# Optimization experiments

Measured on AMD Instinct MI355X. Metric: run time of the kernel, lower is better.

Reference implementation:

```python
import jax, jax.numpy as jnp
import numpy as np

EPS = 1e-5  # BatchNorm eps (torch default)


def setup_inputs() -> dict:
    key = jax.random.key(0)
    ks = jax.random.split(key, 12)
    C, Ci, B, H, W = 64, 32, 2, 96, 96  # plane, inter_plane=plane//2

    def n(k, shape, s=0.05):
        return jax.random.normal(k, shape, jnp.float32) * s

    return {
        "xA": jax.random.normal(ks[0], (B, C, H, W), jnp.float32),
        "xB": jax.random.normal(ks[1], (B, C, H, W), jnp.float32),
        "Wk": n(ks[2], (Ci, C)), "bk": n(ks[3], (Ci,)),
        "Wv": n(ks[4], (Ci, C)), "bv": n(ks[5], (Ci,)),
        "Wq": n(ks[6], (Ci, C)), "bq": n(ks[7], (Ci,)),
        "Wg": n(ks[8], (Ci, Ci)),  # conv_wg, 1x1 Conv1d, no bias
        "g1_gamma": jnp.ones((Ci,), jnp.float32), "g1_beta": jnp.zeros((Ci,), jnp.float32),
        "g1_mean": jnp.zeros((Ci,), jnp.float32), "g1_var": jnp.ones((Ci,), jnp.float32),
        "Wo": n(ks[9], (C, Ci)), "bo": n(ks[10], (C,)),
        "g2_gamma": jnp.ones((C,), jnp.float32), "g2_beta": jnp.zeros((C,), jnp.float32),
        "g2_mean": jnp.zeros((C,), jnp.float32), "g2_var": jnp.ones((C,), jnp.float32),
    }


def reference(xA, xB, Wk, bk, Wv, bv, Wq, bq, Wg,
              g1_gamma, g1_beta, g1_mean, g1_var,
              Wo, bo, g2_gamma, g2_beta, g2_mean, g2_var):
    B, C, H, W = xB.shape
    N = H * W
    # 1x1 conv2d projections -> [B, Ci, N]
    k = (jnp.einsum('bchw,oc->bohw', xA, Wk) + bk[None, :, None, None]).reshape(B, -1, N)
    v = (jnp.einsum('bchw,oc->bohw', xA, Wv) + bv[None, :, None, None]).reshape(B, -1, N)
    q = (jnp.einsum('bchw,oc->bohw', xB, Wq) + bq[None, :, None, None]).reshape(B, -1, N)
    # AV = softmax(v^T @ q, axis=2)  -> [B, N, N]
    A = jax.nn.softmax(jnp.einsum('bcn,bcm->bnm', v, q), axis=2)
    # k @ AV -> [B, Ci, N]
    av = jnp.einsum('bcn,bnm->bcm', k, A)
    # conv_wg (1x1 conv1d, no bias) + BatchNorm1d (inference form)
    av = jnp.einsum('oc,bcn->bon', Wg, av)
    av = (av - g1_mean[None, :, None]) * (g1_gamma / jnp.sqrt(g1_var + EPS))[None, :, None] + g1_beta[None, :, None]
    av = av.reshape(B, -1, H, W)
    # out: 1x1 conv2d -> plane, BatchNorm2d, residual, relu
    o = jnp.einsum('oc,bchw->bohw', Wo, av) + bo[None, :, None, None]
    o = (o - g2_mean[None, :, None, None]) * (g2_gamma / jnp.sqrt(g2_var + EPS))[None, :, None, None] + g2_beta[None, :, None, None]
    return jax.nn.relu(o + xB)
```

## Files before the change

kernel.cpp:

```cpp
#include <hip/hip_runtime.h>
#include <hip/hip_bf16.h>

#define CI 32
#define CC 64
#define NBATCH 2
#define NPIX 9216
#define NSD 24
#define LOG2E 1.4426950408889634f

typedef __attribute__((ext_vector_type(8))) short s16x8;
typedef __attribute__((ext_vector_type(4))) short s16x4;
typedef __attribute__((ext_vector_type(4))) float f32x4;
typedef __attribute__((ext_vector_type(2))) unsigned int u32x2;
typedef __attribute__((ext_vector_type(4))) unsigned int u32x4;

static __device__ __forceinline__ unsigned cvtpk(float a, float b) {
    unsigned d;
    asm("v_cvt_pk_bf16_f32 %0, %1, %2" : "=v"(d) : "v"(a), "v"(b));
    return d;
}
static __device__ __forceinline__ short f2b(float f) {
    union { float f; unsigned u; } v; v.f = f;
    return (short)((v.u + 0x7FFFu + ((v.u >> 16) & 1u)) >> 16);
}
static __device__ __forceinline__ float b2f(short s) {
    union { unsigned u; float f; } v; v.u = ((unsigned)(unsigned short)s) << 16;
    return v.f;
}
static __device__ __forceinline__ s16x8 asS16x8(u32x4 v) {
    union { u32x4 u; s16x8 s; } c; c.u = v; return c.s;
}

__global__ __launch_bounds__(256) void k_proj(
    const float* __restrict__ xA, const float* __restrict__ xB,
    const float* __restrict__ Wk, const float* __restrict__ bk,
    const float* __restrict__ Wv, const float* __restrict__ bv,
    const float* __restrict__ Wq, const float* __restrict__ bq,
    short* __restrict__ vT, short* __restrict__ qT, short* __restrict__ kC)
{
    int mode = blockIdx.y;
    const float* W    = mode == 0 ? Wk : (mode == 1 ? Wv : Wq);
    const float* bias = mode == 0 ? bk : (mode == 1 ? bv : bq);
    const float* X    = mode == 2 ? xB : xA;

    __shared__ float sW[CI * CC];
    __shared__ float sb[CI];
    __shared__ float spart[3][64][33];
    for (int i = threadIdx.x; i < CI * CC; i += 256) sW[i] = W[i];
    if (threadIdx.x < CI) sb[threadIdx.x] = bias[threadIdx.x];
    __syncthreads();

    int q4 = threadIdx.x >> 6;
    int lp = threadIdx.x & 63;
    int idx = blockIdx.x * 64 + lp;
    int b = idx / NPIX, n = idx % NPIX;

    float acc[CI];
    #pragma unroll
    for (int o = 0; o < CI; o++) acc[o] = 0.f;

    const float* px = X + (size_t)b * CC * NPIX + n;
    #pragma unroll
    for (int cc = 0; cc < 16; cc++) {
        int c = q4 * 16 + cc;
        float x = px[(size_t)c * NPIX];
        #pragma unroll
        for (int o = 0; o < CI; o++) acc[o] += sW[o * CC + c] * x;
    }
    if (q4) {
        #pragma unroll
        for (int o = 0; o < CI; o++) spart[q4 - 1][lp][o] = acc[o];
    }
    __syncthreads();
    if (q4 == 0) {
        #pragma unroll
        for (int o = 0; o < CI; o++)
            acc[o] += spart[0][lp][o] + spart[1][lp][o] + spart[2][lp][o] + sb[o];
        if (mode == 0) {
            #pragma unroll
            for (int o = 0; o < CI; o++)
                kC[((size_t)b * CI + o) * NPIX + n] = f2b(acc[o]);
        } else {
            float sc = (mode == 2) ? LOG2E : 1.0f;
            short* dst = (mode == 1 ? vT : qT) + ((size_t)b * NPIX + n) * CI;
            #pragma unroll
            for (int v4 = 0; v4 < 4; v4++) {
                u32x4 pk;
                #pragma unroll
                for (int j = 0; j < 4; j++)
                    pk[j] = cvtpk(acc[v4 * 8 + 2 * j] * sc, acc[v4 * 8 + 2 * j + 1] * sc);
                ((u32x4*)dst)[v4] = pk;
            }
        }
    }
}

__global__ __launch_bounds__(64) void k_denom(
    const short* __restrict__ vT, const short* __restrict__ qT,
    float* __restrict__ sum_part)
{
    int lane = threadIdx.x;
    int r = lane & 15, g = lane >> 4;
    int b = blockIdx.y;
    int nb = blockIdx.x * 32;

    const short* vb = vT + (size_t)b * NPIX * CI;
    s16x8 a0 = *(const s16x8*)(vb + (size_t)(nb + r) * CI + 8 * g);
    s16x8 a1 = *(const s16x8*)(vb + (size_t)(nb + 16 + r) * CI + 8 * g);

    f32x4 s0 = {0.f, 0.f, 0.f, 0.f}, s1 = {0.f, 0.f, 0.f, 0.f};
    f32x4 z  = {0.f, 0.f, 0.f, 0.f};
    const short* qb = qT + (size_t)b * NPIX * CI;
    int mlo = blockIdx.z * (NPIX / NSD);
    int mhi = mlo + NPIX / NSD;

    s16x8 q0 = *(const s16x8*)(qb + (size_t)(mlo + r) * CI + 8 * g);
    s16x8 q1 = *(const s16x8*)(qb + (size_t)(mlo + 16 + r) * CI + 8 * g);
    for (int m0 = mlo; m0 < mhi; m0 += 32) {
        int np = (m0 + 32 < mhi) ? m0 + 32 : mlo;
        s16x8 nq0 = *(const s16x8*)(qb + (size_t)(np + r) * CI + 8 * g);
        s16x8 nq1 = *(const s16x8*)(qb + (size_t)(np + 16 + r) * CI + 8 * g);

        f32x4 t00 = __builtin_amdgcn_mfma_f32_16x16x32_bf16(a0, q0, z, 0, 0, 0);
        f32x4 t01 = __builtin_amdgcn_mfma_f32_16x16x32_bf16(a0, q1, z, 0, 0, 0);
        f32x4 t10 = __builtin_amdgcn_mfma_f32_16x16x32_bf16(a1, q0, z, 0, 0, 0);
        f32x4 t11 = __builtin_amdgcn_mfma_f32_16x16x32_bf16(a1, q1, z, 0, 0, 0);
        #pragma unroll
        for (int e = 0; e < 4; e++) {
            s0[e] += __builtin_amdgcn_exp2f(t00[e]) + __builtin_amdgcn_exp2f(t01[e]);
            s1[e] += __builtin_amdgcn_exp2f(t10[e]) + __builtin_amdgcn_exp2f(t11[e]);
        }
        q0 = nq0; q1 = nq1;
    }
    #pragma unroll
    for (int mask = 1; mask < 16; mask <<= 1) {
        #pragma unroll
        for (int e = 0; e < 4; e++) {
            s0[e] += __shfl_xor(s0[e], mask, 64);
            s1[e] += __shfl_xor(s1[e], mask, 64);
        }
    }
    if (r == 0) {
        float* sp = sum_part + ((size_t)blockIdx.z * NBATCH + b) * NPIX;
        #pragma unroll
        for (int e = 0; e < 4; e++) {
            sp[nb + 4 * g + e]      = s0[e];
            sp[nb + 16 + 4 * g + e] = s1[e];
        }
    }
}

__global__ __launch_bounds__(256) void k_invd(
    const float* __restrict__ sum_part, float* __restrict__ invd)
{
    int idx = blockIdx.x * 256 + threadIdx.x;
    float s = 0.f;
    #pragma unroll
    for (int zz = 0; zz < NSD; zz++)
        s += sum_part[(size_t)zz * NBATCH * NPIX + idx];
    invd[idx] = 1.0f / s;
}

__global__ __launch_bounds__(256) void k_scale(
    short* __restrict__ kC, const float* __restrict__ invd)
{
    int idx = blockIdx.x * 256 + threadIdx.x;
    int n = idx % NPIX;
    int b = idx / (CI * NPIX);
    kC[idx] = f2b(b2f(kC[idx]) * invd[b * NPIX + n]);
}

__global__ __launch_bounds__(64) void k_attn(
    const short* __restrict__ vT, const short* __restrict__ qT,
    const short* __restrict__ kC, short* __restrict__ avp, int slice)
{
    __shared__ short plds[32][36];
    int lane = threadIdx.x;
    int r = lane & 15, g = lane >> 4;
    int b = blockIdx.y;
    int m0 = blockIdx.x * 32;

    const short* qb = qT + (size_t)b * NPIX * CI;
    s16x8 qb0 = *(const s16x8*)(qb + (size_t)(m0 + r) * CI + 8 * g);
    s16x8 qb1 = *(const s16x8*)(qb + (size_t)(m0 + 16 + r) * CI + 8 * g);

    const short* vb = vT + (size_t)b * NPIX * CI;
    const short* k0 = kC + ((size_t)b * CI + r) * NPIX;
    const short* k1 = k0 + (size_t)16 * NPIX;

    f32x4 acc00 = {0,0,0,0}, acc01 = {0,0,0,0}, acc10 = {0,0,0,0}, acc11 = {0,0,0,0};
    f32x4 z = {0,0,0,0};

    int nlo = blockIdx.z * slice;
    int nhi = nlo + slice;

    s16x8 a0  = *(const s16x8*)(vb + (size_t)(nlo + r) * CI + 8 * g);
    s16x8 a1  = *(const s16x8*)(vb + (size_t)(nlo + 16 + r) * CI + 8 * g);
    s16x8 ka0 = *(const s16x8*)(k0 + nlo + 8 * g);
    s16x8 ka1 = *(const s16x8*)(k1 + nlo + 8 * g);

    for (int n0 = nlo; n0 < nhi; n0 += 32) {
        int np = (n0 + 32 < nhi) ? n0 + 32 : nlo;
        s16x8 na0  = *(const s16x8*)(vb + (size_t)(np + r) * CI + 8 * g);
        s16x8 na1  = *(const s16x8*)(vb + (size_t)(np + 16 + r) * CI + 8 * g);
        s16x8 nka0 = *(const s16x8*)(k0 + np + 8 * g);
        s16x8 nka1 = *(const s16x8*)(k1 + np + 8 * g);

        f32x4 t00 = __builtin_amdgcn_mfma_f32_16x16x32_bf16(a0, qb0, z, 0, 0, 0);
        f32x4 t01 = __builtin_amdgcn_mfma_f32_16x16x32_bf16(a0, qb1, z, 0, 0, 0);
        f32x4 t10 = __builtin_amdgcn_mfma_f32_16x16x32_bf16(a1, qb0, z, 0, 0, 0);
        f32x4 t11 = __builtin_amdgcn_mfma_f32_16x16x32_bf16(a1, qb1, z, 0, 0, 0);

        u32x2 w00 = {cvtpk(__builtin_amdgcn_exp2f(t00[0]), __builtin_amdgcn_exp2f(t00[1])),
                     cvtpk(__builtin_amdgcn_exp2f(t00[2]), __builtin_amdgcn_exp2f(t00[3]))};
        u32x2 w10 = {cvtpk(__builtin_amdgcn_exp2f(t10[0]), __builtin_amdgcn_exp2f(t10[1])),
                     cvtpk(__builtin_amdgcn_exp2f(t10[2]), __builtin_amdgcn_exp2f(t10[3]))};
        u32x2 w01 = {cvtpk(__builtin_amdgcn_exp2f(t01[0]), __builtin_amdgcn_exp2f(t01[1])),
                     cvtpk(__builtin_amdgcn_exp2f(t01[2]), __builtin_amdgcn_exp2f(t01[3]))};
        u32x2 w11 = {cvtpk(__builtin_amdgcn_exp2f(t11[0]), __builtin_amdgcn_exp2f(t11[1])),
                     cvtpk(__builtin_amdgcn_exp2f(t11[2]), __builtin_amdgcn_exp2f(t11[3]))};

        *(u32x2*)&plds[r][4 * g]           = w00;
        *(u32x2*)&plds[r][16 + 4 * g]      = w10;
        *(u32x2*)&plds[16 + r][4 * g]      = w01;
        *(u32x2*)&plds[16 + r][16 + 4 * g] = w11;

        s16x4 l0 = *(const s16x4*)&plds[r][8 * g];
        s16x4 h0 = *(const s16x4*)&plds[r][8 * g + 4];
        s16x4 l1 = *(const s16x4*)&plds[16 + r][8 * g];
        s16x4 h1 = *(const s16x4*)&plds[16 + r][8 * g + 4];
        s16x8 pb0 = {l0[0], l0[1], l0[2], l0[3], h0[0], h0[1], h0[2], h0[3]};
        s16x8 pb1 = {l1[0], l1[1], l1[2], l1[3], h1[0], h1[1], h1[2], h1[3]};

        acc00 = __builtin_amdgcn_mfma_f32_16x16x32_bf16(ka0, pb0, acc00, 0, 0, 0);
        acc10 = __builtin_amdgcn_mfma_f32_16x16x32_bf16(ka1, pb0, acc10, 0, 0, 0);
        acc01 = __builtin_amdgcn_mfma_f32_16x16x32_bf16(ka0, pb1, acc01, 0, 0, 0);
        acc11 = __builtin_amdgcn_mfma_f32_16x16x32_bf16(ka1, pb1, acc11, 0, 0, 0);

        a0 = na0; a1 = na1; ka0 = nka0; ka1 = nka1;
    }

    short* dst = avp + ((size_t)blockIdx.z * NBATCH + b) * NPIX * CI;
    u32x2 o00 = {cvtpk(acc00[0], acc00[1]), cvtpk(acc00[2], acc00[3])};
    u32x2 o10 = {cvtpk(acc10[0], acc10[1]), cvtpk(acc10[2], acc10[3])};
    u32x2 o01 = {cvtpk(acc01[0], acc01[1]), cvtpk(acc01[2], acc01[3])};
    u32x2 o11 = {cvtpk(acc11[0], acc11[1]), cvtpk(acc11[2], acc11[3])};
    *(u32x2*)(dst + (size_t)(m0 + r) * CI + 4 * g)           = o00;
    *(u32x2*)(dst + (size_t)(m0 + r) * CI + 16 + 4 * g)      = o10;
    *(u32x2*)(dst + (size_t)(m0 + 16 + r) * CI + 4 * g)      = o01;
    *(u32x2*)(dst + (size_t)(m0 + 16 + r) * CI + 16 + 4 * g) = o11;
}

__global__ __launch_bounds__(256) void e_red(
    const short* __restrict__ avp, short* __restrict__ av, int nsa)
{
    int idx = blockIdx.x * 256 + threadIdx.x;
    const unsigned* src = (const unsigned*)avp;
    float lo = 0.f, hi = 0.f;
    for (int zz = 0; zz < nsa; zz++) {
        unsigned p = src[(size_t)zz * (NBATCH * NPIX * CI / 2) + idx];
        lo += b2f((short)(p & 0xFFFF));
        hi += b2f((short)(p >> 16));
    }
    ((unsigned*)av)[idx] = cvtpk(lo, hi);
}

__global__ __launch_bounds__(256) void e_fused(
    const short* __restrict__ av,
    const float* __restrict__ Wg,
    const float* __restrict__ g1g, const float* __restrict__ g1b,
    const float* __restrict__ g1m, const float* __restrict__ g1v,
    const float* __restrict__ Wo, const float* __restrict__ bo,
    const float* __restrict__ g2g, const float* __restrict__ g2b,
    const float* __restrict__ g2m, const float* __restrict__ g2v,
    const float* __restrict__ xB, float* __restrict__ out)
{
    __shared__ float s1s[CI], t1s[CI], s2s[CC], t2s[CC];
    __shared__ short sa2[4][16][36];
    int t = threadIdx.x;
    if (t < CC) {
        float s = g2g[t] * rsqrtf(g2v[t] + 1e-5f);
        s2s[t] = s; t2s[t] = g2b[t] - g2m[t] * s + bo[t] * s;
    } else if (t < CC + CI) {
        int o = t - CC;
        float s = g1g[o] * rsqrtf(g1v[o] + 1e-5f);
        s1s[o] = s; t1s[o] = g1b[o] - g1m[o] * s;
    }
    __syncthreads();

    int w = t >> 6, lane = t & 63;
    int r = lane & 15, g = lane >> 4;
    int idx0 = blockIdx.x * 64 + w * 16;
    int b = idx0 / NPIX;
    int mcol = (idx0 % NPIX) + r;

    const float* wg0 = Wg + r * CI + 8 * g;
    const float* wg1 = Wg + (16 + r) * CI + 8 * g;
    float sA = s1s[r], sB = s1s[16 + r];
    u32x4 a1l, a1h;
    #pragma unroll
    for (int j = 0; j < 4; j++) {
        a1l[j] = cvtpk(wg0[2 * j] * sA, wg0[2 * j + 1] * sA);
        a1h[j] = cvtpk(wg1[2 * j] * sB, wg1[2 * j + 1] * sB);
    }
    s16x8 A1lo = asS16x8(a1l), A1hi = asS16x8(a1h);

    s16x8 Bav = *(const s16x8*)(av + (size_t)(idx0 + r) * CI + 8 * g);

    f32x4 z = {0, 0, 0, 0};
    f32x4 d1lo = __builtin_amdgcn_mfma_f32_16x16x32_bf16(A1lo, Bav, z, 0, 0, 0);
    f32x4 d1hi = __builtin_amdgcn_mfma_f32_16x16x32_bf16(A1hi, Bav, z, 0, 0, 0);

    u32x2 plo = {cvtpk(d1lo[0] + t1s[4 * g],     d1lo[1] + t1s[4 * g + 1]),
                 cvtpk(d1lo[2] + t1s[4 * g + 2], d1lo[3] + t1s[4 * g + 3])};
    u32x2 phi = {cvtpk(d1hi[0] + t1s[16 + 4 * g],     d1hi[1] + t1s[16 + 4 * g + 1]),
                 cvtpk(d1hi[2] + t1s[16 + 4 * g + 2], d1hi[3] + t1s[16 + 4 * g + 3])};
    *(u32x2*)&sa2[w][r][4 * g]      = plo;
    *(u32x2*)&sa2[w][r][16 + 4 * g] = phi;

    s16x4 l0 = *(const s16x4*)&sa2[w][r][8 * g];
    s16x4 h0 = *(const s16x4*)&sa2[w][r][8 * g + 4];
    s16x8 B2 = {l0[0], l0[1], l0[2], l0[3], h0[0], h0[1], h0[2], h0[3]};

    #pragma unroll
    for (int h = 0; h < 4; h++) {
        const float* wo = Wo + (size_t)(16 * h + r) * CI + 8 * g;
        float s = s2s[16 * h + r];
        u32x4 aw;
        #pragma unroll
        for (int j = 0; j < 4; j++)
            aw[j] = cvtpk(wo[2 * j] * s, wo[2 * j + 1] * s);
        f32x4 d2 = __builtin_amdgcn_mfma_f32_16x16x32_bf16(asS16x8(aw), B2, z, 0, 0, 0);
        #pragma unroll
        for (int e = 0; e < 4; e++) {
            int ch = 16 * h + 4 * g + e;
            size_t oi = ((size_t)b * CC + ch) * NPIX + mcol;
            float v = d2[e] + t2s[ch] + xB[oi];
            out[oi] = v > 0.f ? v : 0.f;
        }
    }
}

extern "C" void kernel_launch(void* const* d_in, const int* in_sizes, int n_in,
                              void* d_out, int out_size, void* d_ws, size_t ws_size,
                              hipStream_t stream)
{
    const float* xA = (const float*)d_in[0];
    const float* xB = (const float*)d_in[1];
    const float* Wk = (const float*)d_in[2];
    const float* bk = (const float*)d_in[3];
    const float* Wv = (const float*)d_in[4];
    const float* bv = (const float*)d_in[5];
    const float* Wq = (const float*)d_in[6];
    const float* bq = (const float*)d_in[7];
    const float* Wg = (const float*)d_in[8];
    const float* g1g = (const float*)d_in[9];
    const float* g1b = (const float*)d_in[10];
    const float* g1m = (const float*)d_in[11];
    const float* g1v = (const float*)d_in[12];
    const float* Wo = (const float*)d_in[13];
    const float* bo = (const float*)d_in[14];
    const float* g2g = (const float*)d_in[15];
    const float* g2b = (const float*)d_in[16];
    const float* g2m = (const float*)d_in[17];
    const float* g2v = (const float*)d_in[18];
    float* out = (float*)d_out;

    char* ws = (char*)d_ws;
    const size_t SZB = (size_t)NBATCH * NPIX * CI * 2;
    short* vT = (short*)(ws);
    short* qT = (short*)(ws + SZB);
    short* kC = (short*)(ws + 2 * SZB);
    float* invd = (float*)(ws + 3 * SZB);
    char*  region = ws + 3 * SZB + (size_t)NBATCH * NPIX * 4;
    float* sum_part = (float*)region;
    short* avp = (short*)region;
    short* av = vT;

    const size_t base = 3 * SZB + (size_t)NBATCH * NPIX * 4;
    int nsa = (ws_size >= base + (size_t)16 * NBATCH * NPIX * CI * 2) ? 16 : 8;
    int slice = NPIX / nsa;

    k_proj<<<dim3(NBATCH * NPIX / 64, 3), dim3(256), 0, stream>>>(
        xA, xB, Wk, bk, Wv, bv, Wq, bq, vT, qT, kC);
    k_denom<<<dim3(NPIX / 32, NBATCH, NSD), dim3(64), 0, stream>>>(
        vT, qT, sum_part);
    k_invd<<<dim3(NBATCH * NPIX / 256), dim3(256), 0, stream>>>(
        sum_part, invd);
    k_scale<<<dim3(NBATCH * CI * NPIX / 256), dim3(256), 0, stream>>>(
        kC, invd);
    k_attn<<<dim3(NPIX / 32, NBATCH, nsa), dim3(64), 0, stream>>>(
        vT, qT, kC, avp, slice);
    e_red<<<dim3(NBATCH * NPIX * CI / 2 / 256), dim3(256), 0, stream>>>(
        avp, av, nsa);
    e_fused<<<dim3(NBATCH * NPIX / 64), dim3(256), 0, stream>>>(
        av, Wg, g1g, g1b, g1m, g1v, Wo, bo, g2g, g2b, g2m, g2v, xB, out);
}
```

Measured before the change: 127.0 us.

## Fold softmax denominator into MFMA accumulator and drop LDS transpose via permuted kC

Instead of scaling kC by 1/denominator in a separate kernel, the log2 of the denominator is negated and fed as the initial accumulator of the score MFMA, so exp2 directly yields normalized probabilities. kC columns are written in a permuted order so the packed exp2 outputs already match the B-operand layout, removing the LDS round trip for P. Blocks now hold two waves each for k_denom and k_attn. This removes one kernel launch and the LDS traffic, at the cost of an extra small float load per iteration and reliance on the permutation matching the MFMA register layout exactly.

Result: no change. 128.3 us (+1.0%).

```diff
diff --git a/kernel.cpp b/kernel.cpp
--- a/kernel.cpp
+++ b/kernel.cpp
@@ -77,9 +77,13 @@
         for (int o = 0; o < CI; o++)
             acc[o] += spart[0][lp][o] + spart[1][lp][o] + spart[2][lp][o] + sb[o];
         if (mode == 0) {
+            int p = n & 31;
+            int pc = (p < 16) ? ((p >> 2) * 8 + (p & 3))
+                              : (((p - 16) >> 2) * 8 + 4 + (p & 3));
+            int ncol = (n & ~31) + pc;
             #pragma unroll
             for (int o = 0; o < CI; o++)
-                kC[((size_t)b * CI + o) * NPIX + n] = f2b(acc[o]);
+                kC[((size_t)b * CI + o) * NPIX + ncol] = f2b(acc[o]);
         } else {
             float sc = (mode == 2) ? LOG2E : 1.0f;
             short* dst = (mode == 1 ? vT : qT) + ((size_t)b * NPIX + n) * CI;
@@ -95,14 +99,14 @@
     }
 }
 
-__global__ __launch_bounds__(64) void k_denom(
+__global__ __launch_bounds__(128) void k_denom(
     const short* __restrict__ vT, const short* __restrict__ qT,
     float* __restrict__ sum_part)
 {
-    int lane = threadIdx.x;
+    int w = threadIdx.x >> 6, lane = threadIdx.x & 63;
     int r = lane & 15, g = lane >> 4;
     int b = blockIdx.y;
-    int nb = blockIdx.x * 32;
+    int nb = blockIdx.x * 64 + w * 32;
 
     const short* vb = vT + (size_t)b * NPIX * CI;
     s16x8 a0 = *(const s16x8*)(vb + (size_t)(nb + r) * CI + 8 * g);
@@ -150,35 +154,26 @@
     }
 }
 
-__global__ __launch_bounds__(256) void k_invd(
-    const float* __restrict__ sum_part, float* __restrict__ invd)
+__global__ __launch_bounds__(256) void k_l2d(
+    const float* __restrict__ sum_part, float* __restrict__ nl2d)
 {
     int idx = blockIdx.x * 256 + threadIdx.x;
     float s = 0.f;
     #pragma unroll
     for (int zz = 0; zz < NSD; zz++)
         s += sum_part[(size_t)zz * NBATCH * NPIX + idx];
-    invd[idx] = 1.0f / s;
-}
-
-__global__ __launch_bounds__(256) void k_scale(
-    short* __restrict__ kC, const float* __restrict__ invd)
-{
-    int idx = blockIdx.x * 256 + threadIdx.x;
-    int n = idx % NPIX;
-    int b = idx / (CI * NPIX);
-    kC[idx] = f2b(b2f(kC[idx]) * invd[b * NPIX + n]);
-}
-
-__global__ __launch_bounds__(64) void k_attn(
+    nl2d[idx] = -__builtin_amdgcn_logf(s);
+}
+
+__global__ __launch_bounds__(128) void k_attn(
     const short* __restrict__ vT, const short* __restrict__ qT,
-    const short* __restrict__ kC, short* __restrict__ avp, int slice)
-{
-    __shared__ short plds[32][36];
-    int lane = threadIdx.x;
+    const short* __restrict__ kC, const float* __restrict__ nl2d,
+    short* __restrict__ avp, int slice)
+{
+    int w = threadIdx.x >> 6, lane = threadIdx.x & 63;
     int r = lane & 15, g = lane >> 4;
     int b = blockIdx.y;
-    int m0 = blockIdx.x * 32;
+    int m0 = blockIdx.x * 64 + w * 32;
 
     const short* qb = qT + (size_t)b * NPIX * CI;
     s16x8 qb0 = *(const s16x8*)(qb + (size_t)(m0 + r) * CI + 8 * g);
@@ -187,9 +182,9 @@
     const short* vb = vT + (size_t)b * NPIX * CI;
     const short* k0 = kC + ((size_t)b * CI + r) * NPIX;
     const short* k1 = k0 + (size_t)16 * NPIX;
+    const float* nl2 = nl2d + (size_t)b * NPIX;
 
     f32x4 acc00 = {0,0,0,0}, acc01 = {0,0,0,0}, acc10 = {0,0,0,0}, acc11 = {0,0,0,0};
-    f32x4 z = {0,0,0,0};
 
     int nlo = blockIdx.z * slice;
     int nhi = nlo + slice;
@@ -206,31 +201,25 @@
         s16x8 nka0 = *(const s16x8*)(k0 + np + 8 * g);
         s16x8 nka1 = *(const s16x8*)(k1 + np + 8 * g);
 
-        f32x4 t00 = __builtin_amdgcn_mfma_f32_16x16x32_bf16(a0, qb0, z, 0, 0, 0);
-        f32x4 t01 = __builtin_amdgcn_mfma_f32_16x16x32_bf16(a0, qb1, z, 0, 0, 0);
-        f32x4 t10 = __builtin_amdgcn_mfma_f32_16x16x32_bf16(a1, qb0, z, 0, 0, 0);
-        f32x4 t11 = __builtin_amdgcn_mfma_f32_16x16x32_bf16(a1, qb1, z, 0, 0, 0);
-
-        u32x2 w00 = {cvtpk(__builtin_amdgcn_exp2f(t00[0]), __builtin_amdgcn_exp2f(t00[1])),
-                     cvtpk(__builtin_amdgcn_exp2f(t00[2]), __builtin_amdgcn_exp2f(t00[3]))};
-        u32x2 w10 = {cvtpk(__builtin_amdgcn_exp2f(t10[0]), __builtin_amdgcn_exp2f(t10[1])),
-                     cvtpk(__builtin_amdgcn_exp2f(t10[2]), __builtin_amdgcn_exp2f(t10[3]))};
-        u32x2 w01 = {cvtpk(__builtin_amdgcn_exp2f(t01[0]), __builtin_amdgcn_exp2f(t01[1])),
-                     cvtpk(__builtin_amdgcn_exp2f(t01[2]), __builtin_amdgcn_exp2f(t01[3]))};
-        u32x2 w11 = {cvtpk(__builtin_amdgcn_exp2f(t11[0]), __builtin_amdgcn_exp2f(t11[1])),
-                     cvtpk(__builtin_amdgcn_exp2f(t11[2]), __builtin_amdgcn_exp2f(t11[3]))};
-
-        *(u32x2*)&plds[r][4 * g]           = w00;
-        *(u32x2*)&plds[r][16 + 4 * g]      = w10;
-        *(u32x2*)&plds[16 + r][4 * g]      = w01;
-        *(u32x2*)&plds[16 + r][16 + 4 * g] = w11;
-
-        s16x4 l0 = *(const s16x4*)&plds[r][8 * g];
-        s16x4 h0 = *(const s16x4*)&plds[r][8 * g + 4];
-        s16x4 l1 = *(const s16x4*)&plds[16 + r][8 * g];
-        s16x4 h1 = *(const s16x4*)&plds[16 + r][8 * g + 4];
-        s16x8 pb0 = {l0[0], l0[1], l0[2], l0[3], h0[0], h0[1], h0[2], h0[3]};
-        s16x8 pb1 = {l1[0], l1[1], l1[2], l1[3], h1[0], h1[1], h1[2], h1[3]};
+        f32x4 c0 = *(const f32x4*)(nl2 + n0 + 4 * g);
+        f32x4 c1 = *(const f32x4*)(nl2 + n0 + 16 + 4 * g);
+
+        f32x4 t00 = __builtin_amdgcn_mfma_f32_16x16x32_bf16(a0, qb0, c0, 0, 0, 0);
+        f32x4 t01 = __builtin_amdgcn_mfma_f32_16x16x32_bf16(a0, qb1, c0, 0, 0, 0);
+        f32x4 t10 = __builtin_amdgcn_mfma_f32_16x16x32_bf16(a1, qb0, c1, 0, 0, 0);
+        f32x4 t11 = __builtin_amdgcn_mfma_f32_16x16x32_bf16(a1, qb1, c1, 0, 0, 0);
+
+        u32x4 p0, p1;
+        p0[0] = cvtpk(__builtin_amdgcn_exp2f(t00[0]), __builtin_amdgcn_exp2f(t00[1]));
+        p0[1] = cvtpk(__builtin_amdgcn_exp2f(t00[2]), __builtin_amdgcn_exp2f(t00[3]));
+        p0[2] = cvtpk(__builtin_amdgcn_exp2f(t10[0]), __builtin_amdgcn_exp2f(t10[1]));
+        p0[3] = cvtpk(__builtin_amdgcn_exp2f(t10[2]), __builtin_amdgcn_exp2f(t10[3]));
+        p1[0] = cvtpk(__builtin_amdgcn_exp2f(t01[0]), __builtin_amdgcn_exp2f(t01[1]));
+        p1[1] = cvtpk(__builtin_amdgcn_exp2f(t01[2]), __builtin_amdgcn_exp2f(t01[3]));
+        p1[2] = cvtpk(__builtin_amdgcn_exp2f(t11[0]), __builtin_amdgcn_exp2f(t11[1]));
+        p1[3] = cvtpk(__builtin_amdgcn_exp2f(t11[2]), __builtin_amdgcn_exp2f(t11[3]));
+        s16x8 pb0 = asS16x8(p0);
+        s16x8 pb1 = asS16x8(p1);
 
         acc00 = __builtin_amdgcn_mfma_f32_16x16x32_bf16(ka0, pb0, acc00, 0, 0, 0);
         acc10 = __builtin_amdgcn_mfma_f32_16x16x32_bf16(ka1, pb0, acc10, 0, 0, 0);
@@ -371,7 +360,7 @@
     short* vT = (short*)(ws);
     short* qT = (short*)(ws + SZB);
     short* kC = (short*)(ws + 2 * SZB);
-    float* invd = (float*)(ws + 3 * SZB);
+    float* nl2d = (float*)(ws + 3 * SZB);
     char*  region = ws + 3 * SZB + (size_t)NBATCH * NPIX * 4;
     float* sum_part = (float*)region;
     short* avp = (short*)region;
@@ -383,14 +372,12 @@
 
     k_proj<<<dim3(NBATCH * NPIX / 64, 3), dim3(256), 0, stream>>>(
         xA, xB, Wk, bk, Wv, bv, Wq, bq, vT, qT, kC);
-    k_denom<<<dim3(NPIX / 32, NBATCH, NSD), dim3(64), 0, stream>>>(
+    k_denom<<<dim3(NPIX / 64, NBATCH, NSD), dim3(128), 0, stream>>>(
         vT, qT, sum_part);
-    k_invd<<<dim3(NBATCH * NPIX / 256), dim3(256), 0, stream>>>(
-        sum_part, invd);
-    k_scale<<<dim3(NBATCH * CI * NPIX / 256), dim3(256), 0, stream>>>(
-        kC, invd);
-    k_attn<<<dim3(NPIX / 32, NBATCH, nsa), dim3(64), 0, stream>>>(
-        vT, qT, kC, avp, slice);
+    k_l2d<<<dim3(NBATCH * NPIX / 256), dim3(256), 0, stream>>>(
+        sum_part, nl2d);
+    k_attn<<<dim3(NPIX / 64, NBATCH, nsa), dim3(128), 0, stream>>>(
+        vT, qT, kC, nl2d, avp, slice);
     e_red<<<dim3(NBATCH * NPIX * CI / 2 / 256), dim3(256), 0, stream>>>(
         avp, av, nsa);
     e_fused<<<dim3(NBATCH * NPIX / 64), dim3(256), 0, stream>>>(
```
